# Performance work log

Hardware: AMD Instinct MI355X
Metric: run time of the kernel (lower is better)

## Reference

```python
import jax, jax.numpy as jnp
import numpy as np

BLOCK = 32   # sparsity block size
HO = 128     # out_features // BLOCK
WO = 128     # in_features  // BLOCK
N_TOK = 8192 # batch * seq tokens


def setup_inputs() -> dict:
    key = jax.random.key(0)
    k1, k2 = jax.random.split(key)
    gi, gj = np.meshgrid(np.arange(HO), np.arange(WO), indexing='ij')
    layout = ((gi + gj) % 4 == 0)
    ri, ci = np.nonzero(layout)              # block row/col indices (the LUT)
    nnz = len(ri)                            # 4096 nonzero blocks
    x = jax.random.normal(k1, (N_TOK, WO * BLOCK), dtype=jnp.float32)
    w_blocks = jax.random.normal(k2, (nnz, BLOCK, BLOCK), dtype=jnp.float32) * 0.02
    return {
        "x": x,
        "w_blocks": w_blocks,
        "ri": jnp.asarray(ri, jnp.int32),
        "ci": jnp.asarray(ci, jnp.int32),
    }


def reference(x, w_blocks, ri, ci):
    # DSD block-sparse matmul: y = x @ W^T where W is block-sparse.
    # Scatter the value blocks into the dense [out, in] weight (math-identical
    # to the LUT-driven Triton kernel), then one GEMM.
    Wb = jnp.zeros((HO, WO, BLOCK, BLOCK), dtype=w_blocks.dtype)
    Wb = Wb.at[ri, ci].set(w_blocks)
    W = Wb.transpose(0, 2, 1, 3).reshape(HO * BLOCK, WO * BLOCK)  # [out, in]
    return x @ W.T  # [N_TOK, out]
```

## Files before the change

### kernel.cpp

```cpp
#include <hip/hip_runtime.h>
#include <hip/hip_bf16.h>

#define BLOCK 32
#define HO 128
#define WO 128
#define NTOK 8192
#define NFEAT 4096

typedef __attribute__((ext_vector_type(8))) short short8;
typedef __attribute__((ext_vector_type(4))) float f32x4;

__device__ inline unsigned short f2bf(float f) {
    union { float f; unsigned u; } v; v.f = f;
    unsigned r = v.u + 0x7FFFu + ((v.u >> 16) & 1u);
    return (unsigned short)(r >> 16);
}

__device__ __forceinline__ void gld16(const unsigned short* g, unsigned short* l) {
    __builtin_amdgcn_global_load_lds(
        (const __attribute__((address_space(1))) unsigned int*)g,
        (__attribute__((address_space(3))) unsigned int*)l, 16, 0, 0);
}

#define VMCNT(N) asm volatile("s_waitcnt vmcnt(" #N ")" ::: "memory")
#define LGKM0 do { asm volatile("s_waitcnt lgkmcnt(0)" ::: "memory"); \
                   __builtin_amdgcn_sched_barrier(0); } while (0)
#define BAR() __builtin_amdgcn_s_barrier()

__global__ __launch_bounds__(256) void cvt_x(const float* __restrict__ x,
                                             unsigned short* __restrict__ xg) {
    const size_t d8 = ((size_t)blockIdx.x * 256 + threadIdx.x) * 8;
    const int p   = (int)(d8 >> 23);
    const int rem = (int)(d8 & ((1u << 23) - 1));
    const int m   = rem >> 10;
    const int dcs = rem & 1023;
    const int c6  = (dcs & 63) ^ ((m & 4) << 2);
    const int dcol = (dcs & ~63) | c6;
    const int kb = dcol >> 5;
    const int cb = (kb << 2) + ((4 - p) & 3);
    const int f  = (cb << 5) + (dcol & 31);
    const float* src = x + (size_t)m * NFEAT + f;
    const float4 v0 = *(const float4*)src;
    const float4 v1 = *(const float4*)(src + 4);
    short8 u;
    u[0] = (short)f2bf(v0.x); u[1] = (short)f2bf(v0.y);
    u[2] = (short)f2bf(v0.z); u[3] = (short)f2bf(v0.w);
    u[4] = (short)f2bf(v1.x); u[5] = (short)f2bf(v1.y);
    u[6] = (short)f2bf(v1.z); u[7] = (short)f2bf(v1.w);
    *(short8*)(xg + d8) = u;
}

__global__ __launch_bounds__(256) void cvt_w(const float* __restrict__ w,
                                             unsigned short* __restrict__ wg) {
    const size_t d8 = ((size_t)blockIdx.x * 256 + threadIdx.x) * 8;
    const int p   = (int)(d8 >> 20);
    const int rem = (int)(d8 & ((1u << 20) - 1));
    const int n   = rem >> 10;
    const int kcs = rem & 1023;
    const int k6  = (kcs & 63) ^ ((n & 4) << 2);
    const int kcol = (kcs & ~63) | k6;
    const int tt = kcol >> 5, cc = kcol & 31;
    const int ro = p + 4 * (n >> 5), rr = n & 31;
    const int bi = ro * 32 + tt;
    const float* src = w + (size_t)bi * 1024 + rr * 32 + cc;
    const float4 v0 = *(const float4*)src;
    const float4 v1 = *(const float4*)(src + 4);
    short8 u;
    u[0] = (short)f2bf(v0.x); u[1] = (short)f2bf(v0.y);
    u[2] = (short)f2bf(v0.z); u[3] = (short)f2bf(v0.w);
    u[4] = (short)f2bf(v1.x); u[5] = (short)f2bf(v1.y);
    u[6] = (short)f2bf(v1.z); u[7] = (short)f2bf(v1.w);
    *(short8*)(wg + d8) = u;
}

template<int QM>
__device__ __forceinline__ void load_a(short8 (&dst)[4][2], const unsigned short* s,
                                       int wm, int lr, int kb8, int csw) {
#pragma unroll
    for (int i = 0; i < 4; i++)
#pragma unroll
        for (int kk = 0; kk < 2; kk++)
            dst[i][kk] = *(const short8*)&s[(wm * 128 + QM * 64 + i * 16 + lr) * 64
                                            + ((kk * 32 + kb8) ^ csw)];
}
template<int QN>
__device__ __forceinline__ void load_b(short8 (&dst)[2][2], const unsigned short* s,
                                       int wn, int lr, int kb8, int csw) {
#pragma unroll
    for (int j = 0; j < 2; j++)
#pragma unroll
        for (int kk = 0; kk < 2; kk++)
            dst[j][kk] = *(const short8*)&s[(wn * 64 + QN * 32 + j * 16 + lr) * 64
                                            + ((kk * 32 + kb8) ^ csw)];
}
template<int QM, int QN>
__device__ __forceinline__ void mfma_quad(f32x4 (&acc)[8][4], const short8 (&a)[4][2],
                                          const short8 (&b)[2][2]) {
#pragma unroll
    for (int i = 0; i < 4; i++)
#pragma unroll
        for (int j = 0; j < 2; j++)
#pragma unroll
            for (int kk = 0; kk < 2; kk++)
                acc[QM * 4 + i][QN * 2 + j] = __builtin_amdgcn_mfma_f32_16x16x32_bf16(
                    a[i][kk], b[j][kk], acc[QM * 4 + i][QN * 2 + j], 0, 0, 0);
}

__device__ __forceinline__ void stage_half(const unsigned short* gbase,
                                           unsigned short* lbase,
                                           int hf, int tt, int sr, int sc) {
    const int r0 = hf * 128 + sr;
    gld16(gbase + (size_t)r0 * 1024 + tt * 64 + sc, lbase + r0 * 64 + sc);
    gld16(gbase + (size_t)(r0 + 8) * 1024 + tt * 64 + sc, lbase + (r0 + 8) * 64 + sc);
}

__global__ __launch_bounds__(512, 2) void gemm8(
    const unsigned short* __restrict__ xg, const unsigned short* __restrict__ wg,
    float* __restrict__ y)
{
    __shared__ unsigned short As[2][256 * 64];
    __shared__ unsigned short Bs[2][256 * 64];

    const int p     = blockIdx.z;
    const int mbase = blockIdx.x * 256;
    const int nbase = blockIdx.y * 256;
    const unsigned short* Ab = xg + (size_t)p * NTOK * 1024 + (size_t)mbase * 1024;
    const unsigned short* Bb = wg + (size_t)p * 1024 * 1024 + (size_t)nbase * 1024;

    const int t    = threadIdx.x;
    const int lane = t & 63;
    const int wv   = t >> 6;
    const int wm   = wv >> 2, wn = wv & 3;
    const int lr   = lane & 15;
    const int kb8  = (lane >> 4) * 8;
    const int csw  = (lr & 4) << 2;
    const int sr   = wv * 16 + (lane >> 3);
    const int sc   = (lane & 7) * 8;

    f32x4 acc[8][4];
#pragma unroll
    for (int i = 0; i < 8; i++)
#pragma unroll
        for (int j = 0; j < 4; j++)
            acc[i][j] = (f32x4){0.f, 0.f, 0.f, 0.f};

    short8 a0[4][2], a1[4][2], b0[2][2], b1[2][2];

    stage_half(Ab, &As[0][0], 0, 0, sr, sc);
    stage_half(Ab, &As[0][0], 1, 0, sr, sc);
    stage_half(Bb, &Bs[0][0], 0, 0, sr, sc);
    stage_half(Bb, &Bs[0][0], 1, 0, sr, sc);
    stage_half(Ab, &As[1][0], 0, 1, sr, sc);
    VMCNT(2);
    BAR();

    for (int it = 0; it < 8; ++it) {
        const int t1 = 2 * it + 1;
        const int t2 = 2 * it + 2;
        const int t3 = 2 * it + 3;
        const bool more = (it < 7);

        load_a<0>(a0, &As[0][0], wm, lr, kb8, csw);
        load_b<0>(b0, &Bs[0][0], wn, lr, kb8, csw);
        stage_half(Ab, &As[1][0], 1, t1, sr, sc);
        BAR(); LGKM0;
        __builtin_amdgcn_s_setprio(1); mfma_quad<0, 0>(acc, a0, b0); __builtin_amdgcn_s_setprio(0);
        BAR();

        load_a<1>(a1, &As[0][0], wm, lr, kb8, csw);
        stage_half(Bb, &Bs[1][0], 0, t1, sr, sc);
        BAR(); LGKM0;
        __builtin_amdgcn_s_setprio(1); mfma_quad<1, 0>(acc, a1, b0); __builtin_amdgcn_s_setprio(0);
        BAR();

        load_b<1>(b1, &Bs[0][0], wn, lr, kb8, csw);
        stage_half(Bb, &Bs[1][0], 1, t1, sr, sc);
        BAR(); LGKM0;
        __builtin_amdgcn_s_setprio(1); mfma_quad<0, 1>(acc, a0, b1); __builtin_amdgcn_s_setprio(0);
        BAR();

        if (more) stage_half(Ab, &As[0][0], 0, t2, sr, sc);
        BAR();
        __builtin_amdgcn_s_setprio(1); mfma_quad<1, 1>(acc, a1, b1); __builtin_amdgcn_s_setprio(0);
        if (more) VMCNT(2); else VMCNT(0);
        BAR();

        load_a<0>(a0, &As[1][0], wm, lr, kb8, csw);
        load_b<0>(b0, &Bs[1][0], wn, lr, kb8, csw);
        if (more) stage_half(Ab, &As[0][0], 1, t2, sr, sc);
        BAR(); LGKM0;
        __builtin_amdgcn_s_setprio(1); mfma_quad<0, 0>(acc, a0, b0); __builtin_amdgcn_s_setprio(0);
        BAR();

        load_a<1>(a1, &As[1][0], wm, lr, kb8, csw);
        if (more) stage_half(Bb, &Bs[0][0], 0, t2, sr, sc);
        BAR(); LGKM0;
        __builtin_amdgcn_s_setprio(1); mfma_quad<1, 0>(acc, a1, b0); __builtin_amdgcn_s_setprio(0);
        BAR();

        load_b<1>(b1, &Bs[1][0], wn, lr, kb8, csw);
        if (more) stage_half(Bb, &Bs[0][0], 1, t2, sr, sc);
        BAR(); LGKM0;
        __builtin_amdgcn_s_setprio(1); mfma_quad<0, 1>(acc, a0, b1); __builtin_amdgcn_s_setprio(0);
        BAR();

        if (more) stage_half(Ab, &As[1][0], 0, t3, sr, sc);
        BAR();
        __builtin_amdgcn_s_setprio(1); mfma_quad<1, 1>(acc, a1, b1); __builtin_amdgcn_s_setprio(0);
        if (more) VMCNT(2);
        BAR();
    }

#pragma unroll
    for (int i = 0; i < 8; i++) {
#pragma unroll
        for (int q = 0; q < 4; q++) {
            const int row = mbase + wm * 128 + i * 16 + (lane >> 4) * 4 + q;
            float* yrow = y + (size_t)row * NFEAT;
#pragma unroll
            for (int j = 0; j < 4; j++) {
                const int n = nbase + wn * 64 + j * 16 + lr;
                const int feat = (p + 4 * (n >> 5)) * 32 + (n & 31);
                yrow[feat] = acc[i][j][q];
            }
        }
    }
}

#define LDA 72
__global__ __launch_bounds__(256) void bsmm_kernel(
    const float* __restrict__ x, const float* __restrict__ w,
    const int* __restrict__ ci, float* __restrict__ y)
{
    __shared__ unsigned short As[128 * LDA];
    __shared__ unsigned short Bs[128 * LDA];
    __shared__ int cis[32];
    const int p = blockIdx.z, ntile = blockIdx.y, mbase = blockIdx.x * 128;
    const int t = threadIdx.x;
    if (t < 32) cis[t] = ci[p * 32 + t];
    const int lane = t & 63, wv = t >> 6, wm = wv >> 1, wn = wv & 1;
    const int lr = lane & 15, lk = (lane >> 4) * 8;
    const int tr = t >> 4, tc4 = (t & 15) * 4, hh = tc4 >> 5, cc = tc4 & 31;
    f32x4 acc[4][4];
#pragma unroll
    for (int i = 0; i < 4; i++)
#pragma unroll
        for (int j = 0; j < 4; j++) acc[i][j] = (f32x4){0.f, 0.f, 0.f, 0.f};
    __syncthreads();
    for (int ks = 0; ks < 16; ++ks) {
        const int b0 = ks * 2;
        const int fbase = cis[b0 + hh] * 32 + cc;
#pragma unroll
        for (int q = 0; q < 8; ++q) {
            const int row = q * 16 + tr;
            const float4 va = *(const float4*)(x + (size_t)(mbase + row) * NFEAT + fbase);
            ushort4 ua; ua.x = f2bf(va.x); ua.y = f2bf(va.y); ua.z = f2bf(va.z); ua.w = f2bf(va.w);
            *(ushort4*)&As[row * LDA + tc4] = ua;
            const int ablk = row >> 5, rr = row & 31;
            const int ro = p + 4 * (ntile * 4 + ablk);
            const int blkidx = ro * 32 + b0 + hh;
            const float4 vb = *(const float4*)(w + (size_t)blkidx * 1024 + rr * 32 + cc);
            ushort4 ub; ub.x = f2bf(vb.x); ub.y = f2bf(vb.y); ub.z = f2bf(vb.z); ub.w = f2bf(vb.w);
            *(ushort4*)&Bs[row * LDA + tc4] = ub;
        }
        __syncthreads();
#pragma unroll
        for (int kk = 0; kk < 2; ++kk) {
            short8 af[4], bf[4];
#pragma unroll
            for (int i = 0; i < 4; i++) af[i] = *(const short8*)&As[(wm * 64 + i * 16 + lr) * LDA + kk * 32 + lk];
#pragma unroll
            for (int j = 0; j < 4; j++) bf[j] = *(const short8*)&Bs[(wn * 64 + j * 16 + lr) * LDA + kk * 32 + lk];
#pragma unroll
            for (int i = 0; i < 4; i++)
#pragma unroll
                for (int j = 0; j < 4; j++)
                    acc[i][j] = __builtin_amdgcn_mfma_f32_16x16x32_bf16(af[i], bf[j], acc[i][j], 0, 0, 0);
        }
        __syncthreads();
    }
#pragma unroll
    for (int i = 0; i < 4; i++)
#pragma unroll
        for (int q = 0; q < 4; q++) {
            const int row = mbase + wm * 64 + i * 16 + (lane >> 4) * 4 + q;
            float* yrow = y + (size_t)row * NFEAT;
#pragma unroll
            for (int j = 0; j < 4; j++) {
                const int n = ntile * 128 + wn * 64 + j * 16 + lr;
                const int A = n >> 5, rr2 = n & 31;
                yrow[(p + 4 * A) * 32 + rr2] = acc[i][j][q];
            }
        }
}

extern "C" void kernel_launch(void* const* d_in, const int* in_sizes, int n_in,
                              void* d_out, int out_size, void* d_ws, size_t ws_size,
                              hipStream_t stream) {
    const float* x  = (const float*)d_in[0];
    const float* w  = (const float*)d_in[1];
    const int*   ci = (const int*)d_in[3];
    float* y = (float*)d_out;

    const size_t xg_elems = (size_t)4 * NTOK * 1024;
    const size_t wg_elems = (size_t)4 * 1024 * 1024;
    const size_t need = (xg_elems + wg_elems) * 2;

    if (ws_size >= need) {
        unsigned short* xg = (unsigned short*)d_ws;
        unsigned short* wg = xg + xg_elems;
        hipLaunchKernelGGL(cvt_x, dim3(((size_t)4 * NTOK * 1024) / (256 * 8)), dim3(256),
                           0, stream, x, xg);
        hipLaunchKernelGGL(cvt_w, dim3(((size_t)4 * 1024 * 1024) / (256 * 8)), dim3(256),
                           0, stream, w, wg);
        dim3 grid(NTOK / 256, 1024 / 256, 4);
        hipLaunchKernelGGL(gemm8, grid, dim3(512), 0, stream, xg, wg, y);
    } else {
        dim3 grid(NTOK / 128, 8, 4);
        hipLaunchKernelGGL(bsmm_kernel, grid, dim3(256), 0, stream, x, w, ci, y);
    }
}
```

Before: 332.3 us.

## Widen LDS XOR swizzle and stage GEMM epilogue through LDS for vector stores

```diff
diff --git a/kernel.cpp b/kernel.cpp
--- a/kernel.cpp
+++ b/kernel.cpp
@@ -34,7 +34,7 @@
     const int rem = (int)(d8 & ((1u << 23) - 1));
     const int m   = rem >> 10;
     const int dcs = rem & 1023;
-    const int c6  = (dcs & 63) ^ ((m & 4) << 2);
+    const int c6  = (dcs & 63) ^ ((m & 12) << 2);
     const int dcol = (dcs & ~63) | c6;
     const int kb = dcol >> 5;
     const int cb = (kb << 2) + ((4 - p) & 3);
@@ -57,7 +57,7 @@
     const int rem = (int)(d8 & ((1u << 20) - 1));
     const int n   = rem >> 10;
     const int kcs = rem & 1023;
-    const int k6  = (kcs & 63) ^ ((n & 4) << 2);
+    const int k6  = (kcs & 63) ^ ((n & 12) << 2);
     const int kcol = (kcs & ~63) | k6;
     const int tt = kcol >> 5, cc = kcol & 31;
     const int ro = p + 4 * (n >> 5), rr = n & 31;
@@ -118,8 +118,11 @@
     const unsigned short* __restrict__ xg, const unsigned short* __restrict__ wg,
     float* __restrict__ y)
 {
-    __shared__ unsigned short As[2][256 * 64];
-    __shared__ unsigned short Bs[2][256 * 64];
+    __shared__ __align__(16) unsigned char smem[131072];
+    unsigned short* A0 = (unsigned short*)smem;
+    unsigned short* A1 = (unsigned short*)(smem + 32768);
+    unsigned short* B0 = (unsigned short*)(smem + 65536);
+    unsigned short* B1 = (unsigned short*)(smem + 98304);
 
     const int p     = blockIdx.z;
     const int mbase = blockIdx.x * 256;
@@ -133,7 +136,7 @@
     const int wm   = wv >> 2, wn = wv & 3;
     const int lr   = lane & 15;
     const int kb8  = (lane >> 4) * 8;
-    const int csw  = (lr & 4) << 2;
+    const int csw  = (lr & 12) << 2;
     const int sr   = wv * 16 + (lane >> 3);
     const int sc   = (lane & 7) * 8;
 
@@ -146,11 +149,11 @@
 
     short8 a0[4][2], a1[4][2], b0[2][2], b1[2][2];
 
-    stage_half(Ab, &As[0][0], 0, 0, sr, sc);
-    stage_half(Ab, &As[0][0], 1, 0, sr, sc);
-    stage_half(Bb, &Bs[0][0], 0, 0, sr, sc);
-    stage_half(Bb, &Bs[0][0], 1, 0, sr, sc);
-    stage_half(Ab, &As[1][0], 0, 1, sr, sc);
+    stage_half(Ab, A0, 0, 0, sr, sc);
+    stage_half(Ab, A0, 1, 0, sr, sc);
+    stage_half(Bb, B0, 0, 0, sr, sc);
+    stage_half(Bb, B0, 1, 0, sr, sc);
+    stage_half(Ab, A1, 0, 1, sr, sc);
     VMCNT(2);
     BAR();
 
@@ -160,69 +163,86 @@
         const int t3 = 2 * it + 3;
         const bool more = (it < 7);
 
-        load_a<0>(a0, &As[0][0], wm, lr, kb8, csw);
-        load_b<0>(b0, &Bs[0][0], wn, lr, kb8, csw);
-        stage_half(Ab, &As[1][0], 1, t1, sr, sc);
+        load_a<0>(a0, A0, wm, lr, kb8, csw);
+        load_b<0>(b0, B0, wn, lr, kb8, csw);
+        stage_half(Ab, A1, 1, t1, sr, sc);
         BAR(); LGKM0;
         __builtin_amdgcn_s_setprio(1); mfma_quad<0, 0>(acc, a0, b0); __builtin_amdgcn_s_setprio(0);
         BAR();
 
-        load_a<1>(a1, &As[0][0], wm, lr, kb8, csw);
-        stage_half(Bb, &Bs[1][0], 0, t1, sr, sc);
+        load_a<1>(a1, A0, wm, lr, kb8, csw);
+        stage_half(Bb, B1, 0, t1, sr, sc);
         BAR(); LGKM0;
         __builtin_amdgcn_s_setprio(1); mfma_quad<1, 0>(acc, a1, b0); __builtin_amdgcn_s_setprio(0);
         BAR();
 
-        load_b<1>(b1, &Bs[0][0], wn, lr, kb8, csw);
-        stage_half(Bb, &Bs[1][0], 1, t1, sr, sc);
+        load_b<1>(b1, B0, wn, lr, kb8, csw);
+        stage_half(Bb, B1, 1, t1, sr, sc);
         BAR(); LGKM0;
         __builtin_amdgcn_s_setprio(1); mfma_quad<0, 1>(acc, a0, b1); __builtin_amdgcn_s_setprio(0);
         BAR();
 
-        if (more) stage_half(Ab, &As[0][0], 0, t2, sr, sc);
+        if (more) stage_half(Ab, A0, 0, t2, sr, sc);
         BAR();
         __builtin_amdgcn_s_setprio(1); mfma_quad<1, 1>(acc, a1, b1); __builtin_amdgcn_s_setprio(0);
         if (more) VMCNT(2); else VMCNT(0);
         BAR();
 
-        load_a<0>(a0, &As[1][0], wm, lr, kb8, csw);
-        load_b<0>(b0, &Bs[1][0], wn, lr, kb8, csw);
-        if (more) stage_half(Ab, &As[0][0], 1, t2, sr, sc);
+        load_a<0>(a0, A1, wm, lr, kb8, csw);
+        load_b<0>(b0, B1, wn, lr, kb8, csw);
+        if (more) stage_half(Ab, A0, 1, t2, sr, sc);
         BAR(); LGKM0;
         __builtin_amdgcn_s_setprio(1); mfma_quad<0, 0>(acc, a0, b0); __builtin_amdgcn_s_setprio(0);
         BAR();
 
-        load_a<1>(a1, &As[1][0], wm, lr, kb8, csw);
-        if (more) stage_half(Bb, &Bs[0][0], 0, t2, sr, sc);
+        load_a<1>(a1, A1, wm, lr, kb8, csw);
+        if (more) stage_half(Bb, B0, 0, t2, sr, sc);
         BAR(); LGKM0;
         __builtin_amdgcn_s_setprio(1); mfma_quad<1, 0>(acc, a1, b0); __builtin_amdgcn_s_setprio(0);
         BAR();
 
-        load_b<1>(b1, &Bs[1][0], wn, lr, kb8, csw);
-        if (more) stage_half(Bb, &Bs[0][0], 1, t2, sr, sc);
+        load_b<1>(b1, B1, wn, lr, kb8, csw);
+        if (more) stage_half(Bb, B0, 1, t2, sr, sc);
         BAR(); LGKM0;
         __builtin_amdgcn_s_setprio(1); mfma_quad<0, 1>(acc, a0, b1); __builtin_amdgcn_s_setprio(0);
         BAR();
 
-        if (more) stage_half(Ab, &As[1][0], 0, t3, sr, sc);
+        if (more) stage_half(Ab, A1, 0, t3, sr, sc);
         BAR();
         __builtin_amdgcn_s_setprio(1); mfma_quad<1, 1>(acc, a1, b1); __builtin_amdgcn_s_setprio(0);
         if (more) VMCNT(2);
         BAR();
     }
 
-#pragma unroll
-    for (int i = 0; i < 8; i++) {
-#pragma unroll
-        for (int q = 0; q < 4; q++) {
-            const int row = mbase + wm * 128 + i * 16 + (lane >> 4) * 4 + q;
-            float* yrow = y + (size_t)row * NFEAT;
-#pragma unroll
-            for (int j = 0; j < 4; j++) {
-                const int n = nbase + wn * 64 + j * 16 + lr;
-                const int feat = (p + 4 * (n >> 5)) * 32 + (n & 31);
-                yrow[feat] = acc[i][j][q];
-            }
+    float* fs = (float*)smem;
+#pragma unroll
+    for (int h = 0; h < 2; ++h) {
+        BAR();
+        if (wm == h) {
+#pragma unroll
+            for (int i = 0; i < 8; i++)
+#pragma unroll
+                for (int q = 0; q < 4; q++) {
+                    const int row = i * 16 + (lane >> 4) * 4 + q;
+                    const int key = ((row >> 2) & 3) << 4;
+#pragma unroll
+                    for (int j = 0; j < 4; j++) {
+                        const int col = wn * 64 + j * 16 + lr;
+                        fs[row * 256 + (col ^ key)] = acc[i][j][q];
+                    }
+                }
+        }
+        BAR();
+#pragma unroll
+        for (int r8 = 0; r8 < 16; ++r8) {
+            const int row = wv * 16 + r8;
+            const int key = ((row >> 2) & 3) << 4;
+            const int col = lane * 4;
+            f32x4 v = *(const f32x4*)&fs[row * 256 + (col ^ key)];
+            const int gr = mbase + h * 128 + row;
+            const int n  = nbase + col;
+            const int feat = (p + 4 * (n >> 5)) * 32 + (n & 31);
+            *(f32x4*)(y + (size_t)gr * NFEAT + feat) = v;
         }
     }
 }
```

Result: no change. 336.2 us (+1.2%).
